# Performance work log

Hardware: AMD Instinct MI355X
Metric: run time of the kernel (lower is better)

Reference implementation:

```python
import jax, jax.numpy as jnp
import numpy as np

C = 384; NH = 12; HD = C // NH; MLP = int(C * 4.0)
B = 8; T = 12; N = 256; BT = B * T
EPS = 1e-6


def _ln(x):
    # LayerNorm without affine, eps=1e-6
    mu = jnp.mean(x, axis=-1, keepdims=True)
    var = jnp.mean(jnp.square(x - mu), axis=-1, keepdims=True)
    return (x - mu) / jnp.sqrt(var + EPS)


def _attention(x, wqkv, bqkv, wproj, bproj, bias=None):
    b, n, c = x.shape
    qkv = (x @ wqkv.T + bqkv).reshape(b, n, 3, NH, HD)
    q = qkv[:, :, 0].transpose(0, 2, 1, 3)  # [b,h,n,d]
    k = qkv[:, :, 1].transpose(0, 2, 1, 3)
    v = qkv[:, :, 2].transpose(0, 2, 1, 3)
    attn = jnp.einsum('bhnd,bhmd->bhnm', q, k) * (HD ** -0.5)
    if bias is not None:
        attn = attn + bias
    attn = jax.nn.softmax(attn, axis=-1)
    out = jnp.einsum('bhnm,bhmd->bhnd', attn, v).transpose(0, 2, 1, 3).reshape(b, n, c)
    return out @ wproj.T + bproj, attn


def setup_inputs() -> dict:
    key = jax.random.key(0)
    ks = jax.random.split(key, 20)
    s = 0.02
    inp = {
        'x': jax.random.normal(ks[0], (BT, N, C), jnp.float32),
        'c': jax.random.normal(ks[1], (BT, C), jnp.float32),
        'rel_pos_bias': jax.random.normal(ks[2], (1, NH, N, N), jnp.float32) * s,
        'w_adaln': jax.random.normal(ks[3], (9 * C, C), jnp.float32) * s,
        'b_adaln': jnp.zeros((9 * C,), jnp.float32),
        'wqkv_s': jax.random.normal(ks[4], (3 * C, C), jnp.float32) * s,
        'bqkv_s': jnp.zeros((3 * C,), jnp.float32),
        'wproj_s': jax.random.normal(ks[5], (C, C), jnp.float32) * s,
        'bproj_s': jnp.zeros((C,), jnp.float32),
        'wqkv_t': jax.random.normal(ks[6], (3 * C, C), jnp.float32) * s,
        'bqkv_t': jnp.zeros((3 * C,), jnp.float32),
        'wproj_t': jax.random.normal(ks[7], (C, C), jnp.float32) * s,
        'bproj_t': jnp.zeros((C,), jnp.float32),
        'w1': jax.random.normal(ks[8], (MLP, C), jnp.float32) * s,
        'b1': jnp.zeros((MLP,), jnp.float32),
        'w2': jax.random.normal(ks[9], (C, MLP), jnp.float32) * s,
        'b2': jnp.zeros((C,), jnp.float32),
        'T_pred': T,
    }
    return inp


def reference(x, c, rel_pos_bias, w_adaln, b_adaln, wqkv_s, bqkv_s, wproj_s, bproj_s,
              wqkv_t, bqkv_t, wproj_t, bproj_t, w1, b1, w2, b2, T_pred):
    mod = jax.nn.silu(c) @ w_adaln.T + b_adaln  # [BT, 9C]
    (shift_s, scale_s, gate_s, shift_t, scale_t, gate_t,
     shift_mlp, scale_mlp, gate_mlp) = jnp.split(mod, 9, axis=1)

    # spatial attention with adaLN modulate + gate
    x_mod = _ln(x) * (1 + scale_s[:, None]) + shift_s[:, None]
    x_s, attn_map = _attention(x_mod, wqkv_s, bqkv_s, wproj_s, bproj_s, bias=rel_pos_bias)
    x = x + gate_s[:, None] * x_s

    if T_pred > 1:
        bt, n, cdim = x.shape
        b = bt // T_pred
        xt = x.reshape(b, T_pred, n, cdim).transpose(0, 2, 1, 3).reshape(b * n, T_pred, cdim)
        sc = scale_t.reshape(b, 1, T_pred, cdim)
        sh = shift_t.reshape(b, 1, T_pred, cdim)
        gt = gate_t.reshape(b, 1, T_pred, cdim)
        norm_t = _ln(xt).reshape(b, n, T_pred, cdim)
        mod_t = (norm_t * (1 + sc) + sh).reshape(b * n, T_pred, cdim)
        x_t, _ = _attention(mod_t, wqkv_t, bqkv_t, wproj_t, bproj_t)
        x_t = (x_t.reshape(b, n, T_pred, cdim) * gt).transpose(0, 2, 1, 3).reshape(bt, n, cdim)
        x = x + x_t

    # gated MLP with exact (erf) GELU, matching nn.GELU default
    h = _ln(x) * (1 + scale_mlp[:, None]) + shift_mlp[:, None]
    h = jax.nn.gelu(h @ w1.T + b1, approximate=False) @ w2.T + b2
    x = x + gate_mlp[:, None] * h
    return (x, attn_map)
```

## Files before the change

### kernel.cpp

```cpp
#include <hip/hip_runtime.h>
#include <hip/hip_bf16.h>
#include <math.h>

typedef __bf16 bf16;
typedef __bf16 bf16x8 __attribute__((ext_vector_type(8)));
typedef __bf16 bf16x4 __attribute__((ext_vector_type(4)));
typedef float  f32x4  __attribute__((ext_vector_type(4)));

#define C_    384
#define NH_   12
#define HD_   32
#define MLP_  1536
#define B_    8
#define T_    12
#define N_    256
#define BT_   96
#define M_    24576
#define NINE_C 3456
#define QKV_  1152

#define GLOAD16(gptr, lptr)                                                \
  __builtin_amdgcn_global_load_lds(                                       \
      (const __attribute__((address_space(1))) void*)(gptr),              \
      (__attribute__((address_space(3))) void*)(lptr), 16, 0, 0)

__device__ __forceinline__ float wave_sum(float v) {
#pragma unroll
  for (int o = 32; o > 0; o >>= 1) v += __shfl_xor(v, o, 64);
  return v;
}

template <typename TO> __device__ __forceinline__ TO to_out(float v);
template <> __device__ __forceinline__ float to_out<float>(float v) { return v; }
template <> __device__ __forceinline__ bf16  to_out<bf16>(float v)  { return (bf16)v; }

struct F2BArgs {
  const float* src[7];
  bf16* dst[7];
  int n4[7];
};
__global__ __launch_bounds__(256) void k_f2b_all(F2BArgs a) {
  const int seg = blockIdx.y;
  const int i = blockIdx.x * 256 + threadIdx.x;
  if (i < a.n4[seg]) {
    float4 v = ((const float4*)a.src[seg])[i];
    bf16x4 o;
    o[0] = (bf16)v.x; o[1] = (bf16)v.y; o[2] = (bf16)v.z; o[3] = (bf16)v.w;
    ((bf16x4*)a.dst[seg])[i] = o;
  }
}

__global__ __launch_bounds__(384) void k_silu(const float* __restrict__ c,
                                              bf16* __restrict__ out) {
  const int row = blockIdx.x, tid = threadIdx.x;
  float v = 0.f;
  if (row < BT_) {
    float cv = c[row * C_ + tid];
    v = cv / (1.f + __expf(-cv));
  }
  out[row * C_ + tid] = (bf16)v;
}

__global__ __launch_bounds__(256) void k_ln_mod(const float* __restrict__ x,
                                                const float* __restrict__ mod,
                                                bf16* __restrict__ out,
                                                int shift_chunk, int scale_chunk) {
  const int wave = threadIdx.x >> 6, lane = threadIdx.x & 63;
  const int r = blockIdx.x * 4 + wave;
  const float* xr = x + (size_t)r * C_;
  float v[6];
  float s = 0.f, ss = 0.f;
#pragma unroll
  for (int e = 0; e < 6; ++e) { v[e] = xr[lane + 64 * e]; s += v[e]; ss += v[e] * v[e]; }
  s = wave_sum(s); ss = wave_sum(ss);
  const float mean = s * (1.f / C_);
  const float var  = ss * (1.f / C_) - mean * mean;
  const float rs   = rsqrtf(var + 1e-6f);
  const int bt = r >> 8;
  const float* sh = mod + (size_t)bt * NINE_C + shift_chunk * C_;
  const float* sc = mod + (size_t)bt * NINE_C + scale_chunk * C_;
  bf16* orow = out + (size_t)r * C_;
#pragma unroll
  for (int e = 0; e < 6; ++e) {
    int cc = lane + 64 * e;
    orow[cc] = (bf16)((v[e] - mean) * rs * (1.f + sc[cc]) + sh[cc]);
  }
}

__global__ __launch_bounds__(256) void k_ln_mod_t(const float* __restrict__ x,
                                                  const float* __restrict__ mod,
                                                  bf16* __restrict__ out) {
  const int wave = threadIdx.x >> 6, lane = threadIdx.x & 63;
  const int rr = blockIdx.x * 4 + wave;
  const int bn = rr / T_, t = rr - bn * T_;
  const int b = bn >> 8, n = bn & 255;
  const int in_row = (b * T_ + t) * N_ + n;
  const int mrow   = b * T_ + t;
  const float* xr = x + (size_t)in_row * C_;
  float v[6];
  float s = 0.f, ss = 0.f;
#pragma unroll
  for (int e = 0; e < 6; ++e) { v[e] = xr[lane + 64 * e]; s += v[e]; ss += v[e] * v[e]; }
  s = wave_sum(s); ss = wave_sum(ss);
  const float mean = s * (1.f / C_);
  const float var  = ss * (1.f / C_) - mean * mean;
  const float rs   = rsqrtf(var + 1e-6f);
  const float* sh = mod + (size_t)mrow * NINE_C + 3 * C_;
  const float* sc = mod + (size_t)mrow * NINE_C + 4 * C_;
  bf16* orow = out + (size_t)rr * C_;
#pragma unroll
  for (int e = 0; e < 6; ++e) {
    int cc = lane + 64 * e;
    orow[cc] = (bf16)((v[e] - mean) * rs * (1.f + sc[cc]) + sh[cc]);
  }
}

template <typename TO, int EPI>
__global__ __launch_bounds__(256) void mfma_gemm(const bf16* __restrict__ A,
                                                 const bf16* __restrict__ W,
                                                 const float* __restrict__ bias,
                                                 TO* __restrict__ out,
                                                 int M, int N, int K,
                                                 const float* __restrict__ base,
                                                 const float* __restrict__ mod,
                                                 int gc, int ntx) {
  __shared__ bf16 As[128 * 64];
  __shared__ bf16 Bs[128 * 64];
  const int tid = threadIdx.x;
  const int w = tid >> 6, l = tid & 63;
  const int nwg = gridDim.x;
  const int q8 = nwg >> 3, r8 = nwg & 7;
  const int xcd = blockIdx.x & 7, idx = blockIdx.x >> 3;
  const int t = (xcd < r8 ? xcd * (q8 + 1) : r8 * (q8 + 1) + (xcd - r8) * q8) + idx;
  const int m0 = (t / ntx) * 128, n0 = (t % ntx) * 128;
  const int wr = w >> 1, wc = w & 1;
  f32x4 acc[4][4];
#pragma unroll
  for (int mi = 0; mi < 4; ++mi)
#pragma unroll
    for (int nj = 0; nj < 4; ++nj) acc[mi][nj] = (f32x4){0.f, 0.f, 0.f, 0.f};

  const int srow8 = l >> 3;
  const int c8    = l & 7;

  for (int k0 = 0; k0 < K; k0 += 64) {
#pragma unroll
    for (int i = 0; i < 4; ++i) {
      int row = w * 32 + i * 8 + srow8;
      int sc = c8 ^ (row & 7);
      GLOAD16(A + (size_t)(m0 + row) * K + k0 + sc * 8,
              (char*)As + (w * 32 + i * 8) * 128);
      GLOAD16(W + (size_t)(n0 + row) * K + k0 + sc * 8,
              (char*)Bs + (w * 32 + i * 8) * 128);
    }
    __syncthreads();
#pragma unroll
    for (int kt = 0; kt < 2; ++kt) {
      bf16x8 a[4], b[4];
      const int cc = kt * 4 + (l >> 4);
#pragma unroll
      for (int mi = 0; mi < 4; ++mi) {
        int row = wr * 64 + mi * 16 + (l & 15);
        a[mi] = *(const bf16x8*)((const char*)As + row * 128 + ((cc ^ (row & 7)) << 4));
      }
#pragma unroll
      for (int nj = 0; nj < 4; ++nj) {
        int row = wc * 64 + nj * 16 + (l & 15);
        b[nj] = *(const bf16x8*)((const char*)Bs + row * 128 + ((cc ^ (row & 7)) << 4));
      }
#pragma unroll
      for (int mi = 0; mi < 4; ++mi)
#pragma unroll
        for (int nj = 0; nj < 4; ++nj)
          acc[mi][nj] = __builtin_amdgcn_mfma_f32_16x16x32_bf16(a[mi], b[nj], acc[mi][nj], 0, 0, 0);
    }
    __syncthreads();
  }
  const int btc = m0 >> 8;
#pragma unroll
  for (int nj = 0; nj < 4; ++nj) {
    int col = n0 + wc * 64 + nj * 16 + (l & 15);
    float bv = bias[col];
    float gv = 0.f;
    if (EPI == 2) gv = mod[(size_t)btc * NINE_C + gc * C_ + col];
#pragma unroll
    for (int mi = 0; mi < 4; ++mi) {
#pragma unroll
      for (int q = 0; q < 4; ++q) {
        int rrow = m0 + wr * 64 + mi * 16 + (l >> 4) * 4 + q;
        float v = acc[mi][nj][q] + bv;
        if (EPI == 0) {
          out[(size_t)rrow * N + col] = to_out<TO>(v);
        } else if (EPI == 1) {
          v = 0.5f * v * (1.f + erff(v * 0.70710678118654752f));
          out[(size_t)rrow * N + col] = to_out<TO>(v);
        } else if (EPI == 2) {
          ((float*)out)[(size_t)rrow * N + col] =
              base[(size_t)rrow * N + col] + gv * v;
        } else {
          int b = rrow / 3072;
          int rem = rrow - b * 3072;
          int n = rem / 12, tt = rem - n * 12;
          int btd = b * 12 + tt;
          size_t dst = ((size_t)btd * 256 + n) * N + col;
          float g = mod[(size_t)btd * NINE_C + 5 * C_ + col];
          ((float*)out)[dst] += g * v;
        }
      }
    }
  }
}

__global__ __launch_bounds__(256) void k_attn_fused(const bf16* __restrict__ qkv,
                                                    const float* __restrict__ bias,
                                                    float* __restrict__ attn,
                                                    bf16* __restrict__ out) {
  __shared__ bf16 Vt[32 * 256];
  __shared__ bf16 Pl[4][16][260];
  const int blk = blockIdx.x;
  const int bt = blk / NH_, h = blk - bt * NH_;
  const int tid = threadIdx.x;
#pragma unroll
  for (int r = 0; r < 4; ++r) {
    int id = tid + 256 * r;
    int j = id >> 2, c = id & 3;
    bf16x8 vv = *(const bf16x8*)(qkv + (size_t)(bt * N_ + j) * QKV_ + 2 * C_ + h * HD_ + c * 8);
    int kc = j >> 3, ke = j & 7;
#pragma unroll
    for (int i = 0; i < 8; ++i) {
      int d = c * 8 + i;
      *(bf16*)((char*)Vt + d * 512 + ((kc ^ (d & 7)) << 4) + ke * 2) = vv[i];
    }
  }
  const int w = tid >> 6, l = tid & 63;
  const int ln = l & 15, kg = l >> 4;
  const bf16* kbase = qkv + (size_t)bt * N_ * QKV_ + C_ + h * HD_ + kg * 8;
  bf16x8 kfr[16];
#pragma unroll
  for (int nj = 0; nj < 16; ++nj)
    kfr[nj] = *(const bf16x8*)(kbase + (size_t)(nj * 16 + ln) * QKV_);
  __syncthreads();

  const float scale = 0.17677669529663687f;
  const float* bb = bias + (size_t)h * N_ * N_;
  float* Pb = attn + (size_t)blk * N_ * N_;
  const bf16* qbase = qkv + (size_t)bt * N_ * QKV_ + h * HD_ + kg * 8;
  char* Pw = (char*)&Pl[w][0][0];

  for (int g = 0; g < 4; ++g) {
    const int i0 = w * 64 + g * 16;
    bf16x8 aq = *(const bf16x8*)(qbase + (size_t)(i0 + ln) * QKV_);
    f32x4 s[16];
#pragma unroll
    for (int nj = 0; nj < 16; ++nj)
      s[nj] = __builtin_amdgcn_mfma_f32_16x16x32_bf16(aq, kfr[nj], (f32x4){0.f,0.f,0.f,0.f}, 0, 0, 0);
#pragma unroll
    for (int q = 0; q < 4; ++q) {
      const int lr = kg * 4 + q;
      const int row = i0 + lr;
      const float* br = bb + (size_t)row * N_ + ln;
      float v[16];
      float mx = -1e30f;
#pragma unroll
      for (int nj = 0; nj < 16; ++nj) {
        v[nj] = s[nj][q] * scale + br[nj * 16];
        mx = fmaxf(mx, v[nj]);
      }
#pragma unroll
      for (int o = 8; o > 0; o >>= 1) mx = fmaxf(mx, __shfl_xor(mx, o, 64));
      float sum = 0.f;
#pragma unroll
      for (int nj = 0; nj < 16; ++nj) { v[nj] = __expf(v[nj] - mx); sum += v[nj]; }
#pragma unroll
      for (int o = 8; o > 0; o >>= 1) sum += __shfl_xor(sum, o, 64);
      float inv = __frcp_rn(sum);
      float* pr = Pb + (size_t)row * N_ + ln;
#pragma unroll
      for (int nj = 0; nj < 16; ++nj) {
        float p = v[nj] * inv;
        pr[nj * 16] = p;
        *(bf16*)(Pw + lr * 520 + (ln + 16 * nj) * 2) = (bf16)p;
      }
    }
    f32x4 o0 = (f32x4){0.f,0.f,0.f,0.f}, o1 = (f32x4){0.f,0.f,0.f,0.f};
#pragma unroll
    for (int kt = 0; kt < 8; ++kt) {
      bf16x8 a = *(const bf16x8*)(Pw + ln * 520 + kt * 64 + kg * 16);
      int kc = kt * 4 + kg;
      bf16x8 b0 = *(const bf16x8*)((const char*)Vt + (size_t)ln * 512 + ((kc ^ (ln & 7)) << 4));
      bf16x8 b1 = *(const bf16x8*)((const char*)Vt + (size_t)(16 + ln) * 512 + ((kc ^ (ln & 7)) << 4));
      o0 = __builtin_amdgcn_mfma_f32_16x16x32_bf16(a, b0, o0, 0, 0, 0);
      o1 = __builtin_amdgcn_mfma_f32_16x16x32_bf16(a, b1, o1, 0, 0, 0);
    }
#pragma unroll
    for (int q = 0; q < 4; ++q) {
      int row = i0 + kg * 4 + q;
      bf16* orow = out + (size_t)(bt * N_ + row) * C_ + h * HD_;
      orow[ln]      = (bf16)o0[q];
      orow[16 + ln] = (bf16)o1[q];
    }
  }
}

__global__ __launch_bounds__(64) void k_attn_t(const bf16* __restrict__ qkv,
                                               bf16* __restrict__ out) {
  __shared__ float q[T_][HD_], k[T_][HD_], v[T_][HD_];
  const int blk = blockIdx.x;
  const int bn = blk / NH_, h = blk - bn * NH_;
  const int tid = threadIdx.x;
  for (int idx = tid; idx < T_ * 3 * HD_; idx += 64) {
    int t = idx / 96, rem = idx - t * 96;
    int s = rem >> 5, d = rem & 31;
    float val = (float)qkv[(size_t)(bn * T_ + t) * QKV_ + s * C_ + h * HD_ + d];
    if (s == 0) q[t][d] = val;
    else if (s == 1) k[t][d] = val;
    else v[t][d] = val;
  }
  __syncthreads();
  if (tid < T_) {
    const int i = tid;
    float sv[T_];
    float m = -1e30f;
#pragma unroll
    for (int j = 0; j < T_; ++j) {
      float s = 0.f;
#pragma unroll
      for (int d = 0; d < HD_; ++d) s += q[i][d] * k[j][d];
      s *= 0.17677669529663687f;
      sv[j] = s; m = fmaxf(m, s);
    }
    float l = 0.f;
#pragma unroll
    for (int j = 0; j < T_; ++j) { sv[j] = __expf(sv[j] - m); l += sv[j]; }
    const float inv = 1.f / l;
    float o[HD_];
#pragma unroll
    for (int d = 0; d < HD_; ++d) o[d] = 0.f;
#pragma unroll
    for (int j = 0; j < T_; ++j)
#pragma unroll
      for (int d = 0; d < HD_; ++d) o[d] += sv[j] * v[j][d];
    bf16* orow = out + (size_t)(bn * T_ + i) * C_ + h * HD_;
#pragma unroll
    for (int d = 0; d < HD_; ++d) orow[d] = (bf16)(o[d] * inv);
  }
}

extern "C" void kernel_launch(void* const* d_in, const int* in_sizes, int n_in,
                              void* d_out, int out_size, void* d_ws, size_t ws_size,
                              hipStream_t stream) {
  const float* x_in   = (const float*)d_in[0];
  const float* c_in   = (const float*)d_in[1];
  const float* relb   = (const float*)d_in[2];
  const float* w_ada  = (const float*)d_in[3];
  const float* b_ada  = (const float*)d_in[4];
  const float* wqkv_s = (const float*)d_in[5];
  const float* bqkv_s = (const float*)d_in[6];
  const float* wproj_s= (const float*)d_in[7];
  const float* bproj_s= (const float*)d_in[8];
  const float* wqkv_t = (const float*)d_in[9];
  const float* bqkv_t = (const float*)d_in[10];
  const float* wproj_t= (const float*)d_in[11];
  const float* bproj_t= (const float*)d_in[12];
  const float* w1     = (const float*)d_in[13];
  const float* b1     = (const float*)d_in[14];
  const float* w2     = (const float*)d_in[15];
  const float* b2     = (const float*)d_in[16];

  float* Xout = (float*)d_out;
  float* attn = (float*)d_out + (size_t)M_ * C_;

  char* ws = (char*)d_ws;
  float* mod    = (float*)ws;
  bf16*  silu_b = (bf16*)(ws + 1769472);
  bf16*  Wb     = (bf16*)(ws + 1867776);
  bf16*  Bbuf   = (bf16*)(ws + 9240576);
  bf16*  Abuf   = (bf16*)(ws + 28114944);

  bf16* wqkv_s_b  = Wb;
  bf16* wproj_s_b = Wb + 442368;
  bf16* wqkv_t_b  = Wb + 589824;
  bf16* wproj_t_b = Wb + 1032192;
  bf16* w1_b      = Wb + 1179648;
  bf16* w2_b      = Wb + 1769472;
  bf16* wada_b    = Wb + 2359296;

  F2BArgs fa;
  fa.src[0] = wqkv_s;  fa.dst[0] = wqkv_s_b;  fa.n4[0] = 110592;
  fa.src[1] = wproj_s; fa.dst[1] = wproj_s_b; fa.n4[1] = 36864;
  fa.src[2] = wqkv_t;  fa.dst[2] = wqkv_t_b;  fa.n4[2] = 110592;
  fa.src[3] = wproj_t; fa.dst[3] = wproj_t_b; fa.n4[3] = 36864;
  fa.src[4] = w1;      fa.dst[4] = w1_b;      fa.n4[4] = 147456;
  fa.src[5] = w2;      fa.dst[5] = w2_b;      fa.n4[5] = 147456;
  fa.src[6] = w_ada;   fa.dst[6] = wada_b;    fa.n4[6] = 331776;
  k_f2b_all<<<dim3(1296, 7), 256, 0, stream>>>(fa);

  k_silu<<<128, 384, 0, stream>>>(c_in, silu_b);
  mfma_gemm<float, 0><<<27, 256, 0, stream>>>(
      silu_b, wada_b, b_ada, mod, 128, NINE_C, C_, nullptr, nullptr, 0, 27);

  k_ln_mod<<<M_ / 4, 256, 0, stream>>>(x_in, mod, Bbuf, 0, 1);
  mfma_gemm<bf16, 0><<<(QKV_/128)*(M_/128), 256, 0, stream>>>(
      Bbuf, wqkv_s_b, bqkv_s, Abuf, M_, QKV_, C_, nullptr, nullptr, 0, QKV_/128);
  k_attn_fused<<<BT_ * NH_, 256, 0, stream>>>(Abuf, relb, attn, Bbuf);
  mfma_gemm<float, 2><<<(C_/128)*(M_/128), 256, 0, stream>>>(
      Bbuf, wproj_s_b, bproj_s, (float*)Xout, M_, C_, C_, x_in, mod, 2, C_/128);

  k_ln_mod_t<<<M_ / 4, 256, 0, stream>>>(Xout, mod, Bbuf);
  mfma_gemm<bf16, 0><<<(QKV_/128)*(M_/128), 256, 0, stream>>>(
      Bbuf, wqkv_t_b, bqkv_t, Abuf, M_, QKV_, C_, nullptr, nullptr, 0, QKV_/128);
  k_attn_t<<<B_ * N_ * NH_, 64, 0, stream>>>(Abuf, Bbuf);
  mfma_gemm<float, 3><<<(C_/128)*(M_/128), 256, 0, stream>>>(
      Bbuf, wproj_t_b, bproj_t, (float*)Xout, M_, C_, C_, nullptr, mod, 5, C_/128);

  k_ln_mod<<<M_ / 4, 256, 0, stream>>>(Xout, mod, Bbuf, 6, 7);
  mfma_gemm<bf16, 1><<<(MLP_/128)*(M_/128), 256, 0, stream>>>(
      Bbuf, w1_b, b1, Abuf, M_, MLP_, C_, nullptr, nullptr, 0, MLP_/128);
  mfma_gemm<float, 2><<<(C_/128)*(M_/128), 256, 0, stream>>>(
      Abuf, w2_b, b2, (float*)Xout, M_, C_, MLP_, Xout, mod, 8, C_/128);
}
```

Before: 526.1 us.

## Add persistent weight-resident GEMM for K=384 projections

Adds a persistent GEMM kernel in which each workgroup loads its full 128x384 weight slice into LDS once, then loops over a strided set of 128-row A tiles with double-buffered async A loads. It replaces the tiled GEMM for the adaLN, both QKV, both projection and the MLP-up GEMMs, with grids sized to about 252-255 workgroups. The aim is to stop reloading weight tiles for every output tile and to amortize launch and prologue cost. The trade-off is 128KB of LDS per workgroup, so only one workgroup runs per CU, which leaves little latency hiding apart from the double buffering.

```diff
diff --git a/kernel.cpp b/kernel.cpp
--- a/kernel.cpp
+++ b/kernel.cpp
@@ -112,6 +112,141 @@
   for (int e = 0; e < 6; ++e) {
     int cc = lane + 64 * e;
     orow[cc] = (bf16)((v[e] - mean) * rs * (1.f + sc[cc]) + sh[cc]);
+  }
+}
+
+template <typename TO, int EPI>
+__global__ __launch_bounds__(256, 1)
+void gemm_pw(const bf16* __restrict__ A, const bf16* __restrict__ W,
+             const float* __restrict__ bias, TO* __restrict__ out,
+             int MT, int N,
+             const float* __restrict__ base, const float* __restrict__ mod,
+             int gc, int ntx, int ngroups) {
+  extern __shared__ char smem[];
+  char* Ab0 = smem + 98304;
+  char* Ab1 = smem + 114688;
+  const int tid = threadIdx.x;
+  const int w = tid >> 6, l = tid & 63;
+  const int nwg = ntx * ngroups;
+  const int q8 = nwg >> 3, r8 = nwg & 7;
+  const int xcd = blockIdx.x & 7, bidx = blockIdx.x >> 3;
+  const int t = (xcd < r8 ? xcd * (q8 + 1) : r8 * (q8 + 1) + (xcd - r8) * q8) + bidx;
+  const int n0 = (t % ntx) * 128;
+  const int g  = t / ntx;
+  const int nmt = (MT - g + ngroups - 1) / ngroups;
+  const int wr = w >> 1, wc = w & 1;
+
+#pragma unroll
+  for (int j = 0; j < 24; ++j) {
+    int ci = (j * 4 + w) * 64 + l;
+    int r = ci / 48, p = ci - r * 48;
+    int sc = p ^ (r & 7);
+    GLOAD16(W + (size_t)(n0 + r) * 384 + sc * 8, smem + (j * 4 + w) * 1024);
+  }
+  {
+    int mt0 = g;
+#pragma unroll
+    for (int i = 0; i < 4; ++i) {
+      int ci = (i * 4 + w) * 64 + l;
+      int r = ci >> 3, p = ci & 7;
+      int sc = p ^ (r & 7);
+      GLOAD16(A + (size_t)(mt0 * 128 + r) * 384 + sc * 8, Ab0 + (i * 4 + w) * 1024);
+    }
+  }
+
+  f32x4 acc[4][4];
+  const int total = nmt * 6;
+  for (int s = 0; s < total; ++s) {
+    const int ti = s / 6, k = s - ti * 6;
+    const int mt = g + ti * ngroups;
+    if (s + 1 < total) {
+      const int s2 = s + 1;
+      const int ti2 = s2 / 6, k2 = s2 - ti2 * 6;
+      const int mt2 = g + ti2 * ngroups;
+      char* dst = (s2 & 1) ? Ab1 : Ab0;
+#pragma unroll
+      for (int i = 0; i < 4; ++i) {
+        int ci = (i * 4 + w) * 64 + l;
+        int r = ci >> 3, p = ci & 7;
+        int sc = p ^ (r & 7);
+        GLOAD16(A + (size_t)(mt2 * 128 + r) * 384 + k2 * 64 + sc * 8,
+                dst + (i * 4 + w) * 1024);
+      }
+      asm volatile("s_waitcnt vmcnt(4)" ::: "memory");
+    } else {
+      asm volatile("s_waitcnt vmcnt(0)" ::: "memory");
+    }
+    __builtin_amdgcn_s_barrier();
+    asm volatile("" ::: "memory");
+
+    if (k == 0) {
+#pragma unroll
+      for (int mi = 0; mi < 4; ++mi)
+#pragma unroll
+        for (int nj = 0; nj < 4; ++nj) acc[mi][nj] = (f32x4){0.f, 0.f, 0.f, 0.f};
+    }
+    const char* Ac = (s & 1) ? Ab1 : Ab0;
+#pragma unroll
+    for (int kt = 0; kt < 2; ++kt) {
+      bf16x8 a[4], b[4];
+      const int cc = kt * 4 + (l >> 4);
+      const int gch = k * 8 + cc;
+#pragma unroll
+      for (int mi = 0; mi < 4; ++mi) {
+        int row = wr * 64 + mi * 16 + (l & 15);
+        a[mi] = *(const bf16x8*)(Ac + row * 128 + ((cc ^ (row & 7)) << 4));
+      }
+#pragma unroll
+      for (int nj = 0; nj < 4; ++nj) {
+        int row = wc * 64 + nj * 16 + (l & 15);
+        b[nj] = *(const bf16x8*)(smem + row * 768 + ((gch ^ (row & 7)) << 4));
+      }
+#pragma unroll
+      for (int mi = 0; mi < 4; ++mi)
+#pragma unroll
+        for (int nj = 0; nj < 4; ++nj)
+          acc[mi][nj] = __builtin_amdgcn_mfma_f32_16x16x32_bf16(a[mi], b[nj], acc[mi][nj], 0, 0, 0);
+    }
+
+    if (k == 5) {
+      const int m0 = mt * 128;
+      const int btc = m0 >> 8;
+#pragma unroll
+      for (int nj = 0; nj < 4; ++nj) {
+        int col = n0 + wc * 64 + nj * 16 + (l & 15);
+        float bv = bias[col];
+        float gv = 0.f;
+        if (EPI == 2) gv = mod[(size_t)btc * NINE_C + gc * C_ + col];
+#pragma unroll
+        for (int mi = 0; mi < 4; ++mi) {
+#pragma unroll
+          for (int q = 0; q < 4; ++q) {
+            int rrow = m0 + wr * 64 + mi * 16 + (l >> 4) * 4 + q;
+            float v = acc[mi][nj][q] + bv;
+            if (EPI == 0) {
+              out[(size_t)rrow * N + col] = to_out<TO>(v);
+            } else if (EPI == 1) {
+              v = 0.5f * v * (1.f + erff(v * 0.70710678118654752f));
+              out[(size_t)rrow * N + col] = to_out<TO>(v);
+            } else if (EPI == 2) {
+              ((float*)out)[(size_t)rrow * N + col] =
+                  base[(size_t)rrow * N + col] + gv * v;
+            } else {
+              int b2 = rrow / 3072;
+              int rem = rrow - b2 * 3072;
+              int n = rem / 12, tt = rem - n * 12;
+              int btd = b2 * 12 + tt;
+              size_t dst = ((size_t)btd * 256 + n) * N + col;
+              float g2 = mod[(size_t)btd * NINE_C + 5 * C_ + col];
+              ((float*)out)[dst] += g2 * v;
+            }
+          }
+        }
+      }
+    }
+    asm volatile("" ::: "memory");
+    __builtin_amdgcn_s_barrier();
+    asm volatile("" ::: "memory");
   }
 }
 
@@ -385,6 +520,19 @@
   bf16* w2_b      = Wb + 1769472;
   bf16* wada_b    = Wb + 2359296;
 
+  {
+    auto* f0 = gemm_pw<float, 0>;
+    auto* f1 = gemm_pw<bf16, 0>;
+    auto* f2 = gemm_pw<float, 2>;
+    auto* f3 = gemm_pw<float, 3>;
+    auto* f4 = gemm_pw<bf16, 1>;
+    hipFuncSetAttribute((const void*)f0, hipFuncAttributeMaxDynamicSharedMemorySize, 131072);
+    hipFuncSetAttribute((const void*)f1, hipFuncAttributeMaxDynamicSharedMemorySize, 131072);
+    hipFuncSetAttribute((const void*)f2, hipFuncAttributeMaxDynamicSharedMemorySize, 131072);
+    hipFuncSetAttribute((const void*)f3, hipFuncAttributeMaxDynamicSharedMemorySize, 131072);
+    hipFuncSetAttribute((const void*)f4, hipFuncAttributeMaxDynamicSharedMemorySize, 131072);
+  }
+
   F2BArgs fa;
   fa.src[0] = wqkv_s;  fa.dst[0] = wqkv_s_b;  fa.n4[0] = 110592;
   fa.src[1] = wproj_s; fa.dst[1] = wproj_s_b; fa.n4[1] = 36864;
@@ -396,26 +544,26 @@
   k_f2b_all<<<dim3(1296, 7), 256, 0, stream>>>(fa);
 
   k_silu<<<128, 384, 0, stream>>>(c_in, silu_b);
-  mfma_gemm<float, 0><<<27, 256, 0, stream>>>(
-      silu_b, wada_b, b_ada, mod, 128, NINE_C, C_, nullptr, nullptr, 0, 27);
+  gemm_pw<float, 0><<<27, 256, 131072, stream>>>(
+      silu_b, wada_b, b_ada, mod, 1, NINE_C, nullptr, nullptr, 0, 27, 1);
 
   k_ln_mod<<<M_ / 4, 256, 0, stream>>>(x_in, mod, Bbuf, 0, 1);
-  mfma_gemm<bf16, 0><<<(QKV_/128)*(M_/128), 256, 0, stream>>>(
-      Bbuf, wqkv_s_b, bqkv_s, Abuf, M_, QKV_, C_, nullptr, nullptr, 0, QKV_/128);
+  gemm_pw<bf16, 0><<<9 * 28, 256, 131072, stream>>>(
+      Bbuf, wqkv_s_b, bqkv_s, Abuf, M_ / 128, QKV_, nullptr, nullptr, 0, 9, 28);
   k_attn_fused<<<BT_ * NH_, 256, 0, stream>>>(Abuf, relb, attn, Bbuf);
-  mfma_gemm<float, 2><<<(C_/128)*(M_/128), 256, 0, stream>>>(
-      Bbuf, wproj_s_b, bproj_s, (float*)Xout, M_, C_, C_, x_in, mod, 2, C_/128);
+  gemm_pw<float, 2><<<3 * 85, 256, 131072, stream>>>(
+      Bbuf, wproj_s_b, bproj_s, (float*)Xout, M_ / 128, C_, x_in, mod, 2, 3, 85);
 
   k_ln_mod_t<<<M_ / 4, 256, 0, stream>>>(Xout, mod, Bbuf);
-  mfma_gemm<bf16, 0><<<(QKV_/128)*(M_/128), 256, 0, stream>>>(
-      Bbuf, wqkv_t_b, bqkv_t, Abuf, M_, QKV_, C_, nullptr, nullptr, 0, QKV_/128);
+  gemm_pw<bf16, 0><<<9 * 28, 256, 131072, stream>>>(
+      Bbuf, wqkv_t_b, bqkv_t, Abuf, M_ / 128, QKV_, nullptr, nullptr, 0, 9, 28);
   k_attn_t<<<B_ * N_ * NH_, 64, 0, stream>>>(Abuf, Bbuf);
-  mfma_gemm<float, 3><<<(C_/128)*(M_/128), 256, 0, stream>>>(
-      Bbuf, wproj_t_b, bproj_t, (float*)Xout, M_, C_, C_, nullptr, mod, 5, C_/128);
+  gemm_pw<float, 3><<<3 * 85, 256, 131072, stream>>>(
+      Bbuf, wproj_t_b, bproj_t, (float*)Xout, M_ / 128, C_, nullptr, mod, 5, 3, 85);
 
   k_ln_mod<<<M_ / 4, 256, 0, stream>>>(Xout, mod, Bbuf, 6, 7);
-  mfma_gemm<bf16, 1><<<(MLP_/128)*(M_/128), 256, 0, stream>>>(
-      Bbuf, w1_b, b1, Abuf, M_, MLP_, C_, nullptr, nullptr, 0, MLP_/128);
+  gemm_pw<bf16, 1><<<12 * 21, 256, 131072, stream>>>(
+      Bbuf, w1_b, b1, Abuf, M_ / 128, MLP_, nullptr, nullptr, 0, 12, 21);
   mfma_gemm<float, 2><<<(C_/128)*(M_/128), 256, 0, stream>>>(
       Abuf, w2_b, b2, (float*)Xout, M_, C_, MLP_, Xout, mod, 8, C_/128);
 }
```

Result: slower. 581.6 us (+10.6%).
